# Optimization experiments

Hardware: AMD Instinct MI355X
Metric: run time of the kernel (lower is better)

Reference implementation:

```python
import jax, jax.numpy as jnp
import numpy as np

BS, T, Q, HID, PROJ = 16, 16, 100, 256, 256


def setup_inputs() -> dict:
    key = jax.random.key(0)
    k1, k2, k3, k4, k5 = jax.random.split(key, 5)
    frame_embeds = jax.random.normal(k1, (BS, T, Q, HID), jnp.float32)
    other_frame_embeds = jax.random.normal(k2, (BS, T, Q, HID), jnp.float32)
    W = jax.random.normal(k3, (HID, PROJ), jnp.float32) / np.sqrt(HID).astype(np.float32)
    b = jax.random.normal(k4, (PROJ,), jnp.float32) * 0.01
    n = BS * Q
    mid = jax.random.randint(k5, (n, 1), 1, T - 1, dtype=jnp.int32)
    bridge = jnp.concatenate(
        [jnp.zeros((n, 1), jnp.int32), mid, jnp.full((n, 1), T - 1, jnp.int32)], axis=1
    )  # (n,3): head=0, random pivot in [1,T-2], tail=T-1
    return {"frame_embeds": frame_embeds, "other_frame_embeds": other_frame_embeds,
            "W": W, "b": b, "bridge": bridge}


def _prep(fe, W, b):
    # Linear proj, (bs,t,q,c)->(bs*q, t, c), L2-normalize per embedding.
    bs, t, q, _ = fe.shape
    x = fe @ W + b
    x = x.transpose(0, 2, 1, 3).reshape(bs * q, t, -1)
    return x / jnp.linalg.norm(x, axis=-1, keepdims=True)


def _forward(frame_embeds, other_frame_embeds, W, b, bridge, delta=0.3):
    cur = _prep(frame_embeds, W, b)      # (n,t,c)
    other = _prep(other_frame_embeds, W, b)
    bh = bridge[:, 0].astype(jnp.float32)
    bp_f = bridge[:, 1].astype(jnp.float32)
    bt = bridge[:, 2].astype(jnp.float32)
    alpha = (bp_f - bh) / (bt - bh)      # (n,)
    sigma = alpha * (bt - bp_f)          # (n,)
    g = jnp.take_along_axis(cur, bridge[:, :, None], axis=1)  # (n,3,c) head/pivot/tail
    # positive brownian-bridge distance
    x = g[:, 1] - (1.0 - alpha)[:, None] * g[:, 0] - alpha[:, None] * g[:, 2]
    numer = jnp.exp(-jnp.sum(x * x, axis=-1) / (2.0 * sigma ** 2))  # (n,)
    # negatives: pivot frame taken from every sequence in [cur; other].
    # ||m_ij - a_i||^2 = ||m_ij||^2 - 2 m_ij.a_i + ||a_i||^2 with m_ij = neg_all[j, bp_i],
    # avoiding the (n,N,3,c) repeat tensor of the original.
    neg_all = jnp.concatenate([cur, other], axis=0)            # (N,t,c)
    a = (1.0 - alpha)[:, None] * g[:, 0] + alpha[:, None] * g[:, 2]  # (n,c)
    cross = jnp.einsum('ic,jtc->ijt', a, neg_all)              # (n,N,t)
    bp = bridge[:, 1]
    cross_g = jnp.take_along_axis(cross, bp[:, None, None], axis=2)[..., 0]  # (n,N)
    nn2_g = jnp.sum(neg_all * neg_all, axis=-1).T[bp]          # (n,N)
    x2 = nn2_g - 2.0 * cross_g + jnp.sum(a * a, axis=-1)[:, None]
    dist = -x2 / (2.0 * sigma ** 2)[:, None]                   # (n,N)
    n = dist.shape[0]
    idx = jnp.arange(n)
    self_dist = dist[idx, idx]
    dist = dist.at[idx, idx].set(-10000.0)
    topv, _ = jax.lax.top_k(dist, 5)
    deno = jnp.exp(jnp.concatenate([self_dist[:, None], topv], axis=-1))  # (n,6)
    brownian_loss = (numer / deno.sum(axis=-1)).mean()
    score = jnp.einsum('nc,nc->n', cur[:, 0], cur[:, -1])
    head_tail_match = jax.nn.softplus(delta - score).mean()
    return brownian_loss, head_tail_match


def reference(frame_embeds, other_frame_embeds, W, b, bridge):
    return _forward(frame_embeds, other_frame_embeds, W, b, bridge)
```

## Files before the change

### kernel.cpp

```cpp
#include <hip/hip_runtime.h>
#include <hip/hip_bf16.h>

#define NROW 1600
#define NEG  3200
#define ROWS_FLAT 25600
#define NSPLIT 25

using bf16x8 = __attribute__((ext_vector_type(8))) short;
using f32x4  = __attribute__((ext_vector_type(4))) float;

__device__ __forceinline__ float bf2f(unsigned v) { return __uint_as_float(v << 16); }
__device__ __forceinline__ ushort f2bf(float f) {
  __hip_bfloat16 h = __float2bfloat16(f);
  return *(ushort*)&h;
}
__device__ __forceinline__ float load1(const ushort* p, size_t idx, int f32) {
  return f32 ? ((const float*)p)[idx] : bf2f(p[idx]);
}
__device__ __forceinline__ void load8(const ushort* p, size_t idx, int f32, float* o) {
  if (f32) {
    const float* q = (const float*)p;
    float4 a = *(const float4*)(q + idx);
    float4 b = *(const float4*)(q + idx + 4);
    o[0]=a.x; o[1]=a.y; o[2]=a.z; o[3]=a.w;
    o[4]=b.x; o[5]=b.y; o[6]=b.z; o[7]=b.w;
  } else {
    uint4 u = *(const uint4*)(p + idx);
    o[0]=bf2f(u.x & 0xffffu); o[1]=bf2f(u.x >> 16);
    o[2]=bf2f(u.y & 0xffffu); o[3]=bf2f(u.y >> 16);
    o[4]=bf2f(u.z & 0xffffu); o[5]=bf2f(u.z >> 16);
    o[6]=bf2f(u.w & 0xffffu); o[7]=bf2f(u.w >> 16);
  }
}
__device__ __forceinline__ int sniff_f32(const ushort* p, int lane) {
  unsigned e = ((unsigned)p[2*lane] >> 7) & 0xffu;
  unsigned long long b = __ballot(e >= 100u && e <= 140u);
  return (__popcll(b) >= 40) ? 0 : 1;
}

__global__ __launch_bounds__(256) void k_prep(const ushort* __restrict__ W,
    const ushort* __restrict__ fe0, const ushort* __restrict__ fe1,
    ushort* __restrict__ Wt, ushort* __restrict__ Xb, int* __restrict__ zbase) {
  const int tid = threadIdx.x;
  if (blockIdx.x == 0 && tid < 21) zbase[tid] = 0;
  if (blockIdx.x < 256) {
    int fW = sniff_f32(W, tid & 63);
    Wt[blockIdx.x * 256 + tid] = f2bf(load1(W, (size_t)tid * 256 + blockIdx.x, fW));
  }
  int r = blockIdx.x * 8 + (tid >> 5);
  int src1 = (r >= ROWS_FLAT);
  const ushort* src = src1 ? fe1 : fe0;
  int rr = src1 ? r - ROWS_FLAT : r;
  int f = sniff_f32(src, tid & 63);
  float o[8];
  load8(src, (size_t)rr * 256 + (size_t)(tid & 31) * 8, f, o);
  int b  = rr / 1600;
  int rm = rr - b * 1600;
  int t  = rm / 100;
  int q  = rm - t * 100;
  int I  = src1 * 1600 + b * 100 + q;
  uint4 u;
  u.x = (unsigned)f2bf(o[0]) | ((unsigned)f2bf(o[1]) << 16);
  u.y = (unsigned)f2bf(o[2]) | ((unsigned)f2bf(o[3]) << 16);
  u.z = (unsigned)f2bf(o[4]) | ((unsigned)f2bf(o[5]) << 16);
  u.w = (unsigned)f2bf(o[6]) | ((unsigned)f2bf(o[7]) << 16);
  *(uint4*)&Xb[((size_t)I * 16 + t) * 256 + (size_t)(tid & 31) * 8] = u;
}

__global__ __launch_bounds__(256) void k_proj(const ushort* __restrict__ Xb,
    const ushort* __restrict__ Wt, const ushort* __restrict__ bias,
    const int* __restrict__ bridge, ushort* __restrict__ Pb,
    ushort* __restrict__ Ab, float* __restrict__ prm, float* __restrict__ numer,
    int* __restrict__ cnt, int* __restrict__ lst, float* __restrict__ wsum) {
  __shared__ union {
    ushort x[64*256];
    ushort c[4][32*72];
  } sh;
  __shared__ float s_ss[4][64];
  __shared__ float s_bb[2][4][2][3];
  __shared__ int   s_brg[4][3];
  const int tid = threadIdx.x;
  const int w = tid >> 6, lane = tid & 63, q = lane >> 4, m = lane & 15;
  const int grow0 = blockIdx.x * 64;
  const int hasB = (blockIdx.x < 400);
  const size_t rbase = (size_t)grow0 * 256;
  const int fB = sniff_f32(bias, lane);
  if (hasB && tid < 12) s_brg[tid / 3][tid % 3] = bridge[(blockIdx.x * 4 + tid / 3) * 3 + tid % 3];
  #pragma unroll
  for (int i = 0; i < 8; i++) {
    int c = w*8 + i;
    int r = 2*c + (lane >> 5);
    int kc = (lane & 31) ^ (r & 7);
    const ushort* gp = Xb + rbase + (size_t)r*256 + kc*8;
    __builtin_amdgcn_global_load_lds(
      (const __attribute__((address_space(1))) unsigned int*)gp,
      (__attribute__((address_space(3))) unsigned int*)&sh.x[c*512],
      16, 0, 0);
  }
  __syncthreads();
  f32x4 acc[4][4];
  #pragma unroll
  for (int nt = 0; nt < 4; nt++) {
    float bb = load1(bias, w*64 + nt*16 + m, fB);
    f32x4 v = {bb, bb, bb, bb};
    #pragma unroll
    for (int mt = 0; mt < 4; mt++) acc[mt][nt] = v;
  }
  const int sw = (m & 7) << 3;
  const ushort* wbase = Wt + (size_t)(w*64 + m)*256 + q*8;
  bf16x8 a_cur[4], b_cur[4];
  #pragma unroll
  for (int mt = 0; mt < 4; mt++)
    a_cur[mt] = *(const bf16x8*)&sh.x[(mt*16 + m)*256 + ((q*8) ^ sw)];
  #pragma unroll
  for (int nt = 0; nt < 4; nt++)
    b_cur[nt] = *(const bf16x8*)(wbase + (size_t)nt*16*256);
  #pragma unroll
  for (int k = 0; k < 8; k++) {
    bf16x8 a_nxt[4], b_nxt[4];
    if (k < 7) {
      int k0 = (k + 1) * 32;
      #pragma unroll
      for (int nt = 0; nt < 4; nt++)
        b_nxt[nt] = *(const bf16x8*)(wbase + (size_t)nt*16*256 + k0);
      int pk = (k0 + q*8) ^ sw;
      #pragma unroll
      for (int mt = 0; mt < 4; mt++)
        a_nxt[mt] = *(const bf16x8*)&sh.x[(mt*16 + m)*256 + pk];
    }
    #pragma unroll
    for (int nt = 0; nt < 4; nt++)
      #pragma unroll
      for (int mt = 0; mt < 4; mt++)
        acc[mt][nt] = __builtin_amdgcn_mfma_f32_16x16x32_bf16(a_cur[mt], b_cur[nt], acc[mt][nt], 0, 0, 0);
    if (k < 7) {
      #pragma unroll
      for (int x = 0; x < 4; x++) { a_cur[x] = a_nxt[x]; b_cur[x] = b_nxt[x]; }
    }
  }
  float ssp[4][4];
  #pragma unroll
  for (int mt = 0; mt < 4; mt++)
    #pragma unroll
    for (int reg = 0; reg < 4; reg++) {
      float s = 0.f;
      #pragma unroll
      for (int nt = 0; nt < 4; nt++) { float v = acc[mt][nt][reg]; s += v*v; }
      ssp[mt][reg] = s;
    }
  #pragma unroll
  for (int mk = 1; mk < 16; mk <<= 1)
    #pragma unroll
    for (int mt = 0; mt < 4; mt++)
      #pragma unroll
      for (int reg = 0; reg < 4; reg++) ssp[mt][reg] += __shfl_xor(ssp[mt][reg], mk, 64);
  if (m == 0)
    #pragma unroll
    for (int mt = 0; mt < 4; mt++)
      #pragma unroll
      for (int reg = 0; reg < 4; reg++) s_ss[w][mt*16 + 4*q + reg] = ssp[mt][reg];
  __syncthreads();
  float inv[4][4];
  #pragma unroll
  for (int mt = 0; mt < 4; mt++)
    #pragma unroll
    for (int reg = 0; reg < 4; reg++) {
      int row = mt*16 + 4*q + reg;
      float s = s_ss[0][row] + s_ss[1][row] + s_ss[2][row] + s_ss[3][row];
      inv[mt][reg] = 1.0f / sqrtf(s);
    }
  #pragma unroll
  for (int half = 0; half < 2; half++) {
    #pragma unroll
    for (int mt = half*2; mt < half*2 + 2; mt++)
      #pragma unroll
      for (int reg = 0; reg < 4; reg++) {
        int rl = (mt - half*2)*16 + 4*q + reg;
        #pragma unroll
        for (int nt = 0; nt < 4; nt++)
          sh.c[w][rl*72 + nt*16 + m] = f2bf(acc[mt][nt][reg] * inv[mt][reg]);
      }
    int rl = (lane >> 3), c16 = lane & 7;
    #pragma unroll
    for (int it = 0; it < 4; it++) {
      int row = it*8 + rl;
      int r   = half*32 + row;
      int ig  = r >> 4, t = r & 15;
      int I   = blockIdx.x*4 + ig;
      size_t orow = ((size_t)t * NEG + I) * 256;
      uint4 v = *(uint4*)&sh.c[w][row*72 + c16*8];
      *(uint4*)(Pb + orow + w*64 + c16*8) = v;
    }
    if (hasB) {
      #pragma unroll
      for (int ih = 0; ih < 2; ih++) {
        int ig = half*2 + ih;
        int bh = s_brg[ig][0], bp = s_brg[ig][1], bt = s_brg[ig][2];
        float alpha = ((float)bp - (float)bh) / ((float)bt - (float)bh);
        int rb = ih*16;
        float g0 = bf2f(sh.c[w][(rb + bh)*72 + lane]);
        float g1 = bf2f(sh.c[w][(rb + bp)*72 + lane]);
        float g2 = bf2f(sh.c[w][(rb + bt)*72 + lane]);
        float hd = bf2f(sh.c[w][(rb +  0)*72 + lane]);
        float tl = bf2f(sh.c[w][(rb + 15)*72 + lane]);
        float a = (1.0f - alpha) * g0 + alpha * g2;
        float x = g1 - a;
        int I = blockIdx.x*4 + ig;
        Ab[(size_t)I*256 + w*64 + lane] = f2bf(a);
        float xx = x*x, aa = a*a, sc = hd*tl;
        #pragma unroll
        for (int mk = 1; mk < 64; mk <<= 1) {
          xx += __shfl_xor(xx, mk, 64);
          aa += __shfl_xor(aa, mk, 64);
          sc += __shfl_xor(sc, mk, 64);
        }
        if (lane == 0) { s_bb[half][w][ih][0] = xx; s_bb[half][w][ih][1] = aa; s_bb[half][w][ih][2] = sc; }
      }
      __syncthreads();
      if (tid < 2) {
        int ig = half*2 + tid;
        int I = blockIdx.x*4 + ig;
        float XX = s_bb[half][0][tid][0] + s_bb[half][1][tid][0] + s_bb[half][2][tid][0] + s_bb[half][3][tid][0];
        float AA = s_bb[half][0][tid][1] + s_bb[half][1][tid][1] + s_bb[half][2][tid][1] + s_bb[half][3][tid][1];
        float SC = s_bb[half][0][tid][2] + s_bb[half][1][tid][2] + s_bb[half][2][tid][2] + s_bb[half][3][tid][2];
        int bh = s_brg[ig][0], bp = s_brg[ig][1], bt = s_brg[ig][2];
        float alpha = ((float)bp - (float)bh) / ((float)bt - (float)bh);
        float sigma = alpha * ((float)bt - (float)bp);
        float inv2s2 = 1.0f / (2.0f * sigma * sigma);
        prm[I*2+0] = inv2s2;
        prm[I*2+1] = AA;
        numer[I] = expf(-XX * inv2s2);
        float sp = log1pf(expf(0.3f - SC));
        atomicAdd(wsum + 1, sp * (1.0f / 1600.0f));
        int pos = atomicAdd(cnt + bp, 1);
        lst[bp * 1600 + pos] = I;
      }
    }
  }
}

__device__ __forceinline__ void sort5(float* c) {
  #define CE(i,j) { float hi = fmaxf(c[i], c[j]), lo = fminf(c[i], c[j]); c[i]=hi; c[j]=lo; }
  CE(0,1) CE(3,4) CE(2,4) CE(2,3) CE(1,4) CE(0,3) CE(0,2) CE(1,3) CE(1,2)
  #undef CE
}
__device__ __forceinline__ void ins5(float* t, float v) {
  float hi, lo;
  hi = fmaxf(t[0], v); lo = fminf(t[0], v); t[0] = hi; v = lo;
  hi = fmaxf(t[1], v); lo = fminf(t[1], v); t[1] = hi; v = lo;
  hi = fmaxf(t[2], v); lo = fminf(t[2], v); t[2] = hi; v = lo;
  hi = fmaxf(t[3], v); lo = fminf(t[3], v); t[3] = hi; v = lo;
  t[4] = fmaxf(t[4], v);
}

__global__ __launch_bounds__(256) void k_cross(const ushort* __restrict__ Pb,
    const ushort* __restrict__ Ab, const float* __restrict__ prm,
    const int* __restrict__ cnt, const int* __restrict__ lst,
    float* __restrict__ part) {
  int t = blockIdx.z;
  int n_t = min(cnt[t], 1600);
  int i0 = blockIdx.y * 64;
  if (i0 >= n_t) return;
  int j0 = blockIdx.x * 128;
  __shared__ int s_gis[64];
  __shared__ float s_red[4][64][6];
  int tid = threadIdx.x;
  if (tid < 64) {
    int gi = lst[t*1600 + min(i0 + tid, n_t - 1)];
    s_gis[tid] = min(max(gi, 0), NROW - 1);
  }
  __syncthreads();
  const int w = tid >> 6, lane = tid & 63, q = lane >> 4, m = lane & 15;
  const ushort* jp0 = Pb + ((size_t)t * NEG + (j0 + w*32 + m)) * 256 + q*8;
  const ushort* jp1 = jp0 + (size_t)16*256;
  int gi[4];
  const ushort* ip[4];
  #pragma unroll
  for (int it = 0; it < 4; it++) {
    gi[it] = s_gis[it*16 + m];
    ip[it] = Ab + (size_t)gi[it] * 256 + q*8;
  }
  f32x4 acc[2][4];
  #pragma unroll
  for (int jt = 0; jt < 2; jt++)
    #pragma unroll
    for (int it = 0; it < 4; it++) { f32x4 z = {0.f,0.f,0.f,0.f}; acc[jt][it] = z; }
  bf16x8 jc0 = *(const bf16x8*)(jp0);
  bf16x8 jc1 = *(const bf16x8*)(jp1);
  bf16x8 ic[4];
  #pragma unroll
  for (int it = 0; it < 4; it++) ic[it] = *(const bf16x8*)(ip[it]);
  #pragma unroll
  for (int k = 0; k < 8; k++) {
    bf16x8 jn0, jn1, in[4];
    if (k < 7) {
      int o = (k + 1) * 32;
      jn0 = *(const bf16x8*)(jp0 + o);
      jn1 = *(const bf16x8*)(jp1 + o);
      #pragma unroll
      for (int it = 0; it < 4; it++) in[it] = *(const bf16x8*)(ip[it] + o);
    }
    __builtin_amdgcn_s_setprio(1);
    #pragma unroll
    for (int it = 0; it < 4; it++) {
      acc[0][it] = __builtin_amdgcn_mfma_f32_16x16x32_bf16(jc0, ic[it], acc[0][it], 0, 0, 0);
      acc[1][it] = __builtin_amdgcn_mfma_f32_16x16x32_bf16(jc1, ic[it], acc[1][it], 0, 0, 0);
    }
    __builtin_amdgcn_s_setprio(0);
    if (k < 7) { jc0 = jn0; jc1 = jn1;
      #pragma unroll
      for (int it = 0; it < 4; it++) ic[it] = in[it];
    }
  }
  float top[4][5], selfv[4];
  float pi[4], pa[4];
  #pragma unroll
  for (int it = 0; it < 4; it++) {
    pi[it] = prm[gi[it]*2]; pa[it] = prm[gi[it]*2+1];
    selfv[it] = -1e30f;
    #pragma unroll
    for (int k = 0; k < 5; k++) top[it][k] = -1e30f;
  }
  #pragma unroll
  for (int jt = 0; jt < 2; jt++)
    #pragma unroll
    for (int reg = 0; reg < 4; reg++) {
      int j = j0 + w*32 + jt*16 + 4*q + reg;
      #pragma unroll
      for (int it = 0; it < 4; it++) {
        float d = -(1.0f - 2.0f*acc[jt][it][reg] + pa[it]) * pi[it];
        if (j == gi[it]) selfv[it] = d; else ins5(top[it], d);
      }
    }
  #pragma unroll
  for (int mk = 16; mk <= 32; mk <<= 1) {
    #pragma unroll
    for (int it = 0; it < 4; it++) {
      float o[5], c[5];
      #pragma unroll
      for (int k = 0; k < 5; k++) o[k] = __shfl_xor(top[it][k], mk, 64);
      #pragma unroll
      for (int k = 0; k < 5; k++) c[k] = fmaxf(top[it][k], o[4 - k]);
      sort5(c);
      #pragma unroll
      for (int k = 0; k < 5; k++) top[it][k] = c[k];
      selfv[it] = fmaxf(selfv[it], __shfl_xor(selfv[it], mk, 64));
    }
  }
  if (q == 0) {
    #pragma unroll
    for (int it = 0; it < 4; it++) {
      #pragma unroll
      for (int k = 0; k < 5; k++) s_red[w][it*16 + m][k] = top[it][k];
      s_red[w][it*16 + m][5] = selfv[it];
    }
  }
  __syncthreads();
  if (tid < 64 && i0 + tid < n_t) {
    float T[5], S = s_red[0][tid][5];
    #pragma unroll
    for (int k = 0; k < 5; k++) T[k] = s_red[0][tid][k];
    #pragma unroll
    for (int w2 = 1; w2 < 4; w2++) {
      #pragma unroll
      for (int k = 0; k < 5; k++) ins5(T, s_red[w2][tid][k]);
      S = fmaxf(S, s_red[w2][tid][5]);
    }
    float* pp = part + ((size_t)s_gis[tid]*NSPLIT + blockIdx.x) * 6;
    #pragma unroll
    for (int k = 0; k < 5; k++) pp[k] = T[k];
    pp[5] = S;
  }
}

__global__ __launch_bounds__(64) void k_merge(const float* __restrict__ part,
    const float* __restrict__ numer, float* __restrict__ wsum, int* __restrict__ done,
    const ushort* __restrict__ fe0, void* __restrict__ out) {
  int i = blockIdx.x * 64 + threadIdx.x;
  const float* pp = part + (size_t)i * NSPLIT * 6;
  float T[5]; float S = pp[5];
  #pragma unroll
  for (int k = 0; k < 5; k++) T[k] = pp[k];
  #pragma unroll
  for (int s = 1; s < NSPLIT; s++) {
    const float* ps = pp + s*6;
    float v0 = ps[0], v1 = ps[1], v2 = ps[2], v3 = ps[3], v4 = ps[4], v5 = ps[5];
    ins5(T, v0); ins5(T, v1); ins5(T, v2); ins5(T, v3); ins5(T, v4);
    S = fmaxf(S, v5);
  }
  float deno = expf(S);
  #pragma unroll
  for (int k = 0; k < 5; k++) deno += expf(T[k]);
  float local = numer[i] / deno;
  #pragma unroll
  for (int mk = 1; mk < 64; mk <<= 1) local += __shfl_xor(local, mk, 64);
  __shared__ int s_last;
  if (threadIdx.x == 0) {
    atomicAdd(wsum + 0, local * (1.0f / 1600.0f));
    __threadfence();
    s_last = (atomicAdd(done, 1) == 24);
  }
  __syncthreads();
  if (s_last) {
    int f = sniff_f32(fe0, threadIdx.x);
    if (threadIdx.x == 0) {
      __threadfence();
      float brown = __hip_atomic_load(wsum + 0, __ATOMIC_RELAXED, __HIP_MEMORY_SCOPE_AGENT);
      float sp    = __hip_atomic_load(wsum + 1, __ATOMIC_RELAXED, __HIP_MEMORY_SCOPE_AGENT);
      if (f) {
        ((float*)out)[0] = brown;
        ((float*)out)[1] = sp;
      } else {
        ushort* o = (ushort*)out;
        o[0] = f2bf(brown);
        o[1] = f2bf(sp);
      }
    }
  }
}

extern "C" void kernel_launch(void* const* d_in, const int* in_sizes, int n_in,
                              void* d_out, int out_size, void* d_ws, size_t ws_size,
                              hipStream_t stream) {
  const ushort* fe0    = (const ushort*)d_in[0];
  const ushort* fe1    = (const ushort*)d_in[1];
  const ushort* W      = (const ushort*)d_in[2];
  const ushort* bias   = (const ushort*)d_in[3];
  const int*    bridge = (const int*)d_in[4];

  ushort* Pb    = (ushort*)d_ws;
  ushort* Xb    = Pb + 13107200;
  ushort* Ab    = Xb + 13107200;
  ushort* Wt    = Ab + 409600;
  float*  part  = (float*)(Wt + 65536);
  float*  prm   = part + 240000;
  float*  numer = prm + 3200;
  float*  wsum  = numer + 1600;
  int*    cnt   = (int*)(wsum + 4);
  int*    done  = cnt + 16;
  int*    lst   = done + 1;

  k_prep  <<<6400, 256, 0, stream>>>(W, fe0, fe1, Wt, Xb, (int*)wsum);
  k_proj  <<<800, 256, 0, stream>>>(Xb, Wt, bias, bridge, Pb, Ab, prm, numer, cnt, lst, wsum);
  k_cross <<<dim3(NSPLIT, 7, 16), 256, 0, stream>>>(Pb, Ab, prm, cnt, lst, part);
  k_merge <<<25, 64, 0, stream>>>(part, numer, wsum, done, fe0, d_out);
}
```

Measured before the change: 176.0 us.

## Fuse input transpose and bf16 conversion into projection kernel loads

The separate pass that converted and transposed both frame-embedding tensors into a bf16 scratch buffer is removed. The projection kernel now gathers rows straight from the original inputs into LDS, keeping fp32 in LDS and converting to bf16 when building MFMA fragments. This avoids writing and re-reading roughly 50 MB of intermediate data. In exchange the projection kernel stages fp32 in shared memory, which doubles its LDS footprint, and adds conversion work to the inner loop. The Pb store is also restructured to use a block-wide sync with cross-wave reads, and the bridge sync is moved out of the conditional branch.

```diff
diff --git a/kernel.cpp b/kernel.cpp
--- a/kernel.cpp
+++ b/kernel.cpp
@@ -17,62 +17,35 @@
 __device__ __forceinline__ float load1(const ushort* p, size_t idx, int f32) {
   return f32 ? ((const float*)p)[idx] : bf2f(p[idx]);
 }
-__device__ __forceinline__ void load8(const ushort* p, size_t idx, int f32, float* o) {
-  if (f32) {
-    const float* q = (const float*)p;
-    float4 a = *(const float4*)(q + idx);
-    float4 b = *(const float4*)(q + idx + 4);
-    o[0]=a.x; o[1]=a.y; o[2]=a.z; o[3]=a.w;
-    o[4]=b.x; o[5]=b.y; o[6]=b.z; o[7]=b.w;
-  } else {
-    uint4 u = *(const uint4*)(p + idx);
-    o[0]=bf2f(u.x & 0xffffu); o[1]=bf2f(u.x >> 16);
-    o[2]=bf2f(u.y & 0xffffu); o[3]=bf2f(u.y >> 16);
-    o[4]=bf2f(u.z & 0xffffu); o[5]=bf2f(u.z >> 16);
-    o[6]=bf2f(u.w & 0xffffu); o[7]=bf2f(u.w >> 16);
-  }
-}
 __device__ __forceinline__ int sniff_f32(const ushort* p, int lane) {
   unsigned e = ((unsigned)p[2*lane] >> 7) & 0xffu;
   unsigned long long b = __ballot(e >= 100u && e <= 140u);
   return (__popcll(b) >= 40) ? 0 : 1;
 }
+__device__ __forceinline__ bf16x8 cvt8(const float* p) {
+  float4 fa = *(const float4*)p;
+  float4 fb = *(const float4*)(p + 4);
+  bf16x8 r;
+  r[0]=(short)f2bf(fa.x); r[1]=(short)f2bf(fa.y); r[2]=(short)f2bf(fa.z); r[3]=(short)f2bf(fa.w);
+  r[4]=(short)f2bf(fb.x); r[5]=(short)f2bf(fb.y); r[6]=(short)f2bf(fb.z); r[7]=(short)f2bf(fb.w);
+  return r;
+}
 
 __global__ __launch_bounds__(256) void k_prep(const ushort* __restrict__ W,
-    const ushort* __restrict__ fe0, const ushort* __restrict__ fe1,
-    ushort* __restrict__ Wt, ushort* __restrict__ Xb, int* __restrict__ zbase) {
-  const int tid = threadIdx.x;
-  if (blockIdx.x == 0 && tid < 21) zbase[tid] = 0;
-  if (blockIdx.x < 256) {
-    int fW = sniff_f32(W, tid & 63);
-    Wt[blockIdx.x * 256 + tid] = f2bf(load1(W, (size_t)tid * 256 + blockIdx.x, fW));
-  }
-  int r = blockIdx.x * 8 + (tid >> 5);
-  int src1 = (r >= ROWS_FLAT);
-  const ushort* src = src1 ? fe1 : fe0;
-  int rr = src1 ? r - ROWS_FLAT : r;
-  int f = sniff_f32(src, tid & 63);
-  float o[8];
-  load8(src, (size_t)rr * 256 + (size_t)(tid & 31) * 8, f, o);
-  int b  = rr / 1600;
-  int rm = rr - b * 1600;
-  int t  = rm / 100;
-  int q  = rm - t * 100;
-  int I  = src1 * 1600 + b * 100 + q;
-  uint4 u;
-  u.x = (unsigned)f2bf(o[0]) | ((unsigned)f2bf(o[1]) << 16);
-  u.y = (unsigned)f2bf(o[2]) | ((unsigned)f2bf(o[3]) << 16);
-  u.z = (unsigned)f2bf(o[4]) | ((unsigned)f2bf(o[5]) << 16);
-  u.w = (unsigned)f2bf(o[6]) | ((unsigned)f2bf(o[7]) << 16);
-  *(uint4*)&Xb[((size_t)I * 16 + t) * 256 + (size_t)(tid & 31) * 8] = u;
-}
-
-__global__ __launch_bounds__(256) void k_proj(const ushort* __restrict__ Xb,
-    const ushort* __restrict__ Wt, const ushort* __restrict__ bias,
-    const int* __restrict__ bridge, ushort* __restrict__ Pb,
-    ushort* __restrict__ Ab, float* __restrict__ prm, float* __restrict__ numer,
-    int* __restrict__ cnt, int* __restrict__ lst, float* __restrict__ wsum) {
+    ushort* __restrict__ Wt, int* __restrict__ zbase) {
+  if (blockIdx.x == 0 && threadIdx.x < 21) zbase[threadIdx.x] = 0;
+  int fW = sniff_f32(W, threadIdx.x & 63);
+  Wt[blockIdx.x * 256 + threadIdx.x] = f2bf(load1(W, (size_t)threadIdx.x * 256 + blockIdx.x, fW));
+}
+
+__global__ __launch_bounds__(256) void k_proj(const ushort* __restrict__ fe0,
+    const ushort* __restrict__ fe1, const ushort* __restrict__ Wt,
+    const ushort* __restrict__ bias, const int* __restrict__ bridge,
+    ushort* __restrict__ Pb, ushort* __restrict__ Ab, float* __restrict__ prm,
+    float* __restrict__ numer, int* __restrict__ cnt, int* __restrict__ lst,
+    float* __restrict__ wsum) {
   __shared__ union {
+    float  xf[64*256];
     ushort x[64*256];
     ushort c[4][32*72];
   } sh;
@@ -81,21 +54,40 @@
   __shared__ int   s_brg[4][3];
   const int tid = threadIdx.x;
   const int w = tid >> 6, lane = tid & 63, q = lane >> 4, m = lane & 15;
-  const int grow0 = blockIdx.x * 64;
-  const int hasB = (blockIdx.x < 400);
-  const size_t rbase = (size_t)grow0 * 256;
-  const int fB = sniff_f32(bias, lane);
-  if (hasB && tid < 12) s_brg[tid / 3][tid % 3] = bridge[(blockIdx.x * 4 + tid / 3) * 3 + tid % 3];
-  #pragma unroll
-  for (int i = 0; i < 8; i++) {
-    int c = w*8 + i;
-    int r = 2*c + (lane >> 5);
-    int kc = (lane & 31) ^ (r & 7);
-    const ushort* gp = Xb + rbase + (size_t)r*256 + kc*8;
-    __builtin_amdgcn_global_load_lds(
-      (const __attribute__((address_space(1))) unsigned int*)gp,
-      (__attribute__((address_space(3))) unsigned int*)&sh.x[c*512],
-      16, 0, 0);
+  const int I0 = blockIdx.x * 4;
+  const int hasB = (I0 < NROW);
+  const int s1 = (I0 >= NROW);
+  const ushort* srcp = s1 ? fe1 : fe0;
+  const int fSrc = sniff_f32(srcp, lane);
+  const int fB   = sniff_f32(bias, lane);
+  if (hasB && tid < 12) s_brg[tid/3][tid%3] = bridge[(I0 + tid/3)*3 + tid%3];
+  {
+    int ii = I0 - s1*NROW + w;
+    int b = ii / 100, qq = ii - b*100;
+    const size_t ub = (size_t)(b*1600 + qq) * 256;
+    if (fSrc) {
+      const float* fp = (const float*)srcp;
+      #pragma unroll
+      for (int i2 = 0; i2 < 16; i2++) {
+        int r = w*16 + i2;
+        int g = lane ^ ((i2 & 7) << 1);
+        const float* gp = fp + ub + (size_t)i2*25600 + g*4;
+        __builtin_amdgcn_global_load_lds(
+          (const __attribute__((address_space(1))) unsigned int*)gp,
+          (__attribute__((address_space(3))) unsigned int*)&sh.xf[r*256], 16, 0, 0);
+      }
+    } else {
+      #pragma unroll
+      for (int i2 = 0; i2 < 8; i2++) {
+        int c = w*8 + i2;
+        int t  = 2*i2 + (lane >> 5);
+        int kc = (lane & 31) ^ (t & 7);
+        const ushort* gp = srcp + ub + (size_t)t*25600 + kc*8;
+        __builtin_amdgcn_global_load_lds(
+          (const __attribute__((address_space(1))) unsigned int*)gp,
+          (__attribute__((address_space(3))) unsigned int*)&sh.x[c*512], 16, 0, 0);
+      }
+    }
   }
   __syncthreads();
   f32x4 acc[4][4];
@@ -107,11 +99,18 @@
     for (int mt = 0; mt < 4; mt++) acc[mt][nt] = v;
   }
   const int sw = (m & 7) << 3;
+  const int e2 = (m & 7) << 1;
   const ushort* wbase = Wt + (size_t)(w*64 + m)*256 + q*8;
   bf16x8 a_cur[4], b_cur[4];
-  #pragma unroll
-  for (int mt = 0; mt < 4; mt++)
-    a_cur[mt] = *(const bf16x8*)&sh.x[(mt*16 + m)*256 + ((q*8) ^ sw)];
+  if (fSrc) {
+    int pg = (q*2) ^ e2;
+    #pragma unroll
+    for (int mt = 0; mt < 4; mt++) a_cur[mt] = cvt8(&sh.xf[(mt*16 + m)*256 + pg*4]);
+  } else {
+    #pragma unroll
+    for (int mt = 0; mt < 4; mt++)
+      a_cur[mt] = *(const bf16x8*)&sh.x[(mt*16 + m)*256 + ((q*8) ^ sw)];
+  }
   #pragma unroll
   for (int nt = 0; nt < 4; nt++)
     b_cur[nt] = *(const bf16x8*)(wbase + (size_t)nt*16*256);
@@ -123,10 +122,16 @@
       #pragma unroll
       for (int nt = 0; nt < 4; nt++)
         b_nxt[nt] = *(const bf16x8*)(wbase + (size_t)nt*16*256 + k0);
-      int pk = (k0 + q*8) ^ sw;
-      #pragma unroll
-      for (int mt = 0; mt < 4; mt++)
-        a_nxt[mt] = *(const bf16x8*)&sh.x[(mt*16 + m)*256 + pk];
+      if (fSrc) {
+        int pg = ((k+1)*8 + q*2) ^ e2;
+        #pragma unroll
+        for (int mt = 0; mt < 4; mt++) a_nxt[mt] = cvt8(&sh.xf[(mt*16 + m)*256 + pg*4]);
+      } else {
+        int pk = (k0 + q*8) ^ sw;
+        #pragma unroll
+        for (int mt = 0; mt < 4; mt++)
+          a_nxt[mt] = *(const bf16x8*)&sh.x[(mt*16 + m)*256 + pk];
+      }
     }
     #pragma unroll
     for (int nt = 0; nt < 4; nt++)
@@ -180,16 +185,16 @@
         for (int nt = 0; nt < 4; nt++)
           sh.c[w][rl*72 + nt*16 + m] = f2bf(acc[mt][nt][reg] * inv[mt][reg]);
       }
-    int rl = (lane >> 3), c16 = lane & 7;
-    #pragma unroll
-    for (int it = 0; it < 4; it++) {
-      int row = it*8 + rl;
+    __syncthreads();
+    #pragma unroll
+    for (int p = 0; p < 4; p++) {
+      int row = p*8 + (tid >> 5);
       int r   = half*32 + row;
       int ig  = r >> 4, t = r & 15;
-      int I   = blockIdx.x*4 + ig;
-      size_t orow = ((size_t)t * NEG + I) * 256;
-      uint4 v = *(uint4*)&sh.c[w][row*72 + c16*8];
-      *(uint4*)(Pb + orow + w*64 + c16*8) = v;
+      int I   = I0 + ig;
+      int ch  = tid & 31;
+      uint4 v = *(uint4*)&sh.c[ch >> 3][row*72 + (ch & 7)*8];
+      *(uint4*)(Pb + ((size_t)t * NEG + I) * 256 + ch*8) = v;
     }
     if (hasB) {
       #pragma unroll
@@ -205,7 +210,7 @@
         float tl = bf2f(sh.c[w][(rb + 15)*72 + lane]);
         float a = (1.0f - alpha) * g0 + alpha * g2;
         float x = g1 - a;
-        int I = blockIdx.x*4 + ig;
+        int I = I0 + ig;
         Ab[(size_t)I*256 + w*64 + lane] = f2bf(a);
         float xx = x*x, aa = a*a, sc = hd*tl;
         #pragma unroll
@@ -216,25 +221,25 @@
         }
         if (lane == 0) { s_bb[half][w][ih][0] = xx; s_bb[half][w][ih][1] = aa; s_bb[half][w][ih][2] = sc; }
       }
-      __syncthreads();
-      if (tid < 2) {
-        int ig = half*2 + tid;
-        int I = blockIdx.x*4 + ig;
-        float XX = s_bb[half][0][tid][0] + s_bb[half][1][tid][0] + s_bb[half][2][tid][0] + s_bb[half][3][tid][0];
-        float AA = s_bb[half][0][tid][1] + s_bb[half][1][tid][1] + s_bb[half][2][tid][1] + s_bb[half][3][tid][1];
-        float SC = s_bb[half][0][tid][2] + s_bb[half][1][tid][2] + s_bb[half][2][tid][2] + s_bb[half][3][tid][2];
-        int bh = s_brg[ig][0], bp = s_brg[ig][1], bt = s_brg[ig][2];
-        float alpha = ((float)bp - (float)bh) / ((float)bt - (float)bh);
-        float sigma = alpha * ((float)bt - (float)bp);
-        float inv2s2 = 1.0f / (2.0f * sigma * sigma);
-        prm[I*2+0] = inv2s2;
-        prm[I*2+1] = AA;
-        numer[I] = expf(-XX * inv2s2);
-        float sp = log1pf(expf(0.3f - SC));
-        atomicAdd(wsum + 1, sp * (1.0f / 1600.0f));
-        int pos = atomicAdd(cnt + bp, 1);
-        lst[bp * 1600 + pos] = I;
-      }
+    }
+    __syncthreads();
+    if (hasB && tid < 2) {
+      int ig = half*2 + tid;
+      int I = I0 + ig;
+      float XX = s_bb[half][0][tid][0] + s_bb[half][1][tid][0] + s_bb[half][2][tid][0] + s_bb[half][3][tid][0];
+      float AA = s_bb[half][0][tid][1] + s_bb[half][1][tid][1] + s_bb[half][2][tid][1] + s_bb[half][3][tid][1];
+      float SC = s_bb[half][0][tid][2] + s_bb[half][1][tid][2] + s_bb[half][2][tid][2] + s_bb[half][3][tid][2];
+      int bh = s_brg[ig][0], bp = s_brg[ig][1], bt = s_brg[ig][2];
+      float alpha = ((float)bp - (float)bh) / ((float)bt - (float)bh);
+      float sigma = alpha * ((float)bt - (float)bp);
+      float inv2s2 = 1.0f / (2.0f * sigma * sigma);
+      prm[I*2+0] = inv2s2;
+      prm[I*2+1] = AA;
+      numer[I] = expf(-XX * inv2s2);
+      float sp = log1pf(expf(0.3f - SC));
+      atomicAdd(wsum + 1, sp * (1.0f / 1600.0f));
+      int pos = atomicAdd(cnt + bp, 1);
+      lst[bp * 1600 + pos] = I;
     }
   }
 }
@@ -429,8 +434,7 @@
   const int*    bridge = (const int*)d_in[4];
 
   ushort* Pb    = (ushort*)d_ws;
-  ushort* Xb    = Pb + 13107200;
-  ushort* Ab    = Xb + 13107200;
+  ushort* Ab    = Pb + 13107200;
   ushort* Wt    = Ab + 409600;
   float*  part  = (float*)(Wt + 65536);
   float*  prm   = part + 240000;
@@ -440,8 +444,8 @@
   int*    done  = cnt + 16;
   int*    lst   = done + 1;
 
-  k_prep  <<<6400, 256, 0, stream>>>(W, fe0, fe1, Wt, Xb, (int*)wsum);
-  k_proj  <<<800, 256, 0, stream>>>(Xb, Wt, bias, bridge, Pb, Ab, prm, numer, cnt, lst, wsum);
+  k_prep  <<<256, 256, 0, stream>>>(W, Wt, (int*)wsum);
+  k_proj  <<<800, 256, 0, stream>>>(fe0, fe1, Wt, bias, bridge, Pb, Ab, prm, numer, cnt, lst, wsum);
   k_cross <<<dim3(NSPLIT, 7, 16), 256, 0, stream>>>(Pb, Ab, prm, cnt, lst, part);
   k_merge <<<25, 64, 0, stream>>>(part, numer, wsum, done, fe0, d_out);
 }
```

Result: faster. 168.5 us (-4.3%).
